# Performance work log

Hardware: AMD Instinct MI355X
Metric: run time of the kernel (lower is better)

## Reference

```python
import jax, jax.numpy as jnp
import numpy as np

B, H = 65536, 1024


def setup_inputs() -> dict:
    key = jax.random.key(0)
    ks = jax.random.split(key, 8)
    pos = jax.random.normal(ks[0], (B, 3), dtype=jnp.float32)
    quat = jax.random.normal(ks[1], (B, 4), dtype=jnp.float32)
    quat = quat / jnp.linalg.norm(quat, axis=-1, keepdims=True)
    gripper = jax.random.randint(ks[2], (B, 1), 0, 2).astype(jnp.float32)
    actions = jnp.concatenate([pos, quat, gripper], axis=-1)  # (B, 8)
    return {
        "actions": actions,
        "pos_W": jax.random.normal(ks[3], (3, H), dtype=jnp.float32) * 0.02,
        "pos_b": jnp.zeros((H,), dtype=jnp.float32),
        "rot_W": jax.random.normal(ks[4], (6, H), dtype=jnp.float32) * 0.02,
        "rot_b": jnp.zeros((H,), dtype=jnp.float32),
        "open_emb": jax.random.normal(ks[5], (2, H), dtype=jnp.float32) * 0.02,
        "ln_g": jnp.ones((H,), dtype=jnp.float32),
        "ln_b": jnp.zeros((H,), dtype=jnp.float32),
    }


def quat_to_euler_xyz(quat):
    # scipy R.from_quat uses (x, y, z, w); as_euler('xyz') = extrinsic x-y-z
    # (classic roll/pitch/yaw). Normalize like scipy does.
    quat = quat / jnp.linalg.norm(quat, axis=-1, keepdims=True)
    x, y, z, w = quat[..., 0], quat[..., 1], quat[..., 2], quat[..., 3]
    roll = jnp.arctan2(2.0 * (w * x + y * z), 1.0 - 2.0 * (x * x + y * y))
    pitch = jnp.arcsin(jnp.clip(2.0 * (w * y - z * x), -1.0, 1.0))
    yaw = jnp.arctan2(2.0 * (w * z + x * y), 1.0 - 2.0 * (y * y + z * z))
    return jnp.stack([roll, pitch, yaw], axis=-1)


def reference(actions, pos_W, pos_b, rot_W, rot_b, open_emb, ln_g, ln_b):
    pos_embeds = actions[..., :3] @ pos_W + pos_b
    open_idx = actions[..., 7].astype(jnp.int32)
    open_embeds = open_emb[open_idx]
    # original detaches quats (.data.cpu()) before conversion
    eul = quat_to_euler_xyz(jax.lax.stop_gradient(actions[..., 3:7]))
    rot_inputs = jnp.concatenate([jnp.sin(eul), jnp.cos(eul)], axis=-1)  # (B, 6)
    rot_embeds = rot_inputs @ rot_W + rot_b
    h = pos_embeds + rot_embeds + open_embeds
    mu = jnp.mean(h, axis=-1, keepdims=True)
    var = jnp.mean(jnp.square(h - mu), axis=-1, keepdims=True)
    return (h - mu) / jnp.sqrt(var + 1e-12) * ln_g + ln_b
```

## Files before the change

kernel.cpp:

```cpp
#include <hip/hip_runtime.h>
#include <math.h>


#define HDIM 1024
#define TPB  256
#define CPT  4
#define RPB  32

__global__ __launch_bounds__(TPB) void action_embed_kernel(
    const float* __restrict__ actions,
    const float* __restrict__ pos_W, const float* __restrict__ pos_b,
    const float* __restrict__ rot_W, const float* __restrict__ rot_b,
    const float* __restrict__ open_emb,
    const float* __restrict__ ln_g, const float* __restrict__ ln_b,
    float* __restrict__ out, int B)
{
    __shared__ float s_coef[RPB][12];
    __shared__ float s_red[2][4][2];

    const int tid  = threadIdx.x;
    const int col  = tid * CPT;
    const int row0 = blockIdx.x * RPB;

    const float4 wp0 = *(const float4*)(pos_W + 0 * HDIM + col);
    const float4 wp1 = *(const float4*)(pos_W + 1 * HDIM + col);
    const float4 wp2 = *(const float4*)(pos_W + 2 * HDIM + col);
    const float4 wr0 = *(const float4*)(rot_W + 0 * HDIM + col);
    const float4 wr1 = *(const float4*)(rot_W + 1 * HDIM + col);
    const float4 wr2 = *(const float4*)(rot_W + 2 * HDIM + col);
    const float4 wr3 = *(const float4*)(rot_W + 3 * HDIM + col);
    const float4 wr4 = *(const float4*)(rot_W + 4 * HDIM + col);
    const float4 wr5 = *(const float4*)(rot_W + 5 * HDIM + col);
    const float4 wo0 = *(const float4*)(open_emb + 0 * HDIM + col);
    const float4 wo1 = *(const float4*)(open_emb + 1 * HDIM + col);
    float4 bb;
    {
        float4 pb = *(const float4*)(pos_b + col);
        float4 rb = *(const float4*)(rot_b + col);
        bb = make_float4(pb.x + rb.x, pb.y + rb.y, pb.z + rb.z, pb.w + rb.w);
    }
    const float4 g  = *(const float4*)(ln_g + col);
    const float4 bt = *(const float4*)(ln_b + col);

    if (tid < RPB) {
        const int r = row0 + tid;
        if (r < B) {
            const float4 a0 = *(const float4*)(actions + (size_t)r * 8);
            const float4 a1 = *(const float4*)(actions + (size_t)r * 8 + 4);
            float qx = a0.w, qy = a1.x, qz = a1.y, qw = a1.z;
            const float n = 1.0f / sqrtf(qx * qx + qy * qy + qz * qz + qw * qw);
            qx *= n; qy *= n; qz *= n; qw *= n;
            const float sr_n = 2.0f * (qw * qx + qy * qz);
            const float cr_n = 1.0f - 2.0f * (qx * qx + qy * qy);
            float sr, cr;
            {
                const float r2 = sr_n * sr_n + cr_n * cr_n;
                if (r2 < 1e-37f) { sr = 0.0f; cr = 1.0f; }
                else { const float ri = 1.0f / sqrtf(r2); sr = sr_n * ri; cr = cr_n * ri; }
            }
            float sp = 2.0f * (qw * qy - qz * qx);
            sp = fminf(1.0f, fmaxf(-1.0f, sp));
            const float cp = sqrtf(fmaxf(0.0f, 1.0f - sp * sp));
            const float sy_n = 2.0f * (qw * qz + qx * qy);
            const float cy_n = 1.0f - 2.0f * (qy * qy + qz * qz);
            float sy, cy;
            {
                const float r2 = sy_n * sy_n + cy_n * cy_n;
                if (r2 < 1e-37f) { sy = 0.0f; cy = 1.0f; }
                else { const float ri = 1.0f / sqrtf(r2); sy = sy_n * ri; cy = cy_n * ri; }
            }
            s_coef[tid][0] = a0.x;
            s_coef[tid][1] = a0.y;
            s_coef[tid][2] = a0.z;
            s_coef[tid][3] = sr;
            s_coef[tid][4] = sp;
            s_coef[tid][5] = sy;
            s_coef[tid][6] = cr;
            s_coef[tid][7] = cp;
            s_coef[tid][8] = cy;
            int idx = (int)a1.w;
            idx = idx < 0 ? 0 : (idx > 1 ? 1 : idx);
            s_coef[tid][9] = (float)idx;
        }
    }
    __syncthreads();

    const int wave = tid >> 6;
    const int lane = tid & 63;
    const int nrows = (B - row0 < RPB) ? (B - row0) : RPB;

    for (int rr = 0; rr < nrows; ++rr) {
        const float c0 = s_coef[rr][0], c1 = s_coef[rr][1], c2 = s_coef[rr][2];
        const float sr = s_coef[rr][3], sp = s_coef[rr][4], sy = s_coef[rr][5];
        const float cr = s_coef[rr][6], cp = s_coef[rr][7], cy = s_coef[rr][8];
        const bool open = s_coef[rr][9] != 0.0f;

        float4 h;
#define COMPONENT(f)                                                        \
        {                                                                   \
            float hh = bb.f + (open ? wo1.f : wo0.f);                       \
            hh = fmaf(c0, wp0.f, hh);                                       \
            hh = fmaf(c1, wp1.f, hh);                                       \
            hh = fmaf(c2, wp2.f, hh);                                       \
            hh = fmaf(sr, wr0.f, hh);                                       \
            hh = fmaf(sp, wr1.f, hh);                                       \
            hh = fmaf(sy, wr2.f, hh);                                       \
            hh = fmaf(cr, wr3.f, hh);                                       \
            hh = fmaf(cp, wr4.f, hh);                                       \
            hh = fmaf(cy, wr5.f, hh);                                       \
            h.f = hh;                                                       \
        }
        COMPONENT(x) COMPONENT(y) COMPONENT(z) COMPONENT(w)
#undef COMPONENT

        float ps = h.x + h.y + h.z + h.w;
        float pq = h.x * h.x + h.y * h.y + h.z * h.z + h.w * h.w;
        #pragma unroll
        for (int off = 32; off > 0; off >>= 1) {
            ps += __shfl_xor(ps, off, 64);
            pq += __shfl_xor(pq, off, 64);
        }
        const int buf = rr & 1;
        if (lane == 0) {
            s_red[buf][wave][0] = ps;
            s_red[buf][wave][1] = pq;
        }
        __syncthreads();
        const float sum = s_red[buf][0][0] + s_red[buf][1][0] +
                          s_red[buf][2][0] + s_red[buf][3][0];
        const float sq  = s_red[buf][0][1] + s_red[buf][1][1] +
                          s_red[buf][2][1] + s_red[buf][3][1];

        const float mu  = sum * (1.0f / HDIM);
        float var = fmaf(sq, 1.0f / HDIM, -mu * mu);
        var = fmaxf(var, 0.0f);
        const float rstd = 1.0f / sqrtf(var + 1e-12f);

        float4 o;
        o.x = fmaf((h.x - mu) * rstd, g.x, bt.x);
        o.y = fmaf((h.y - mu) * rstd, g.y, bt.y);
        o.z = fmaf((h.z - mu) * rstd, g.z, bt.z);
        o.w = fmaf((h.w - mu) * rstd, g.w, bt.w);
        *(float4*)(out + (size_t)(row0 + rr) * HDIM + col) = o;
    }
}

extern "C" void kernel_launch(void* const* d_in, const int* in_sizes, int n_in,
                              void* d_out, int out_size, void* d_ws, size_t ws_size,
                              hipStream_t stream) {
    const float* actions  = (const float*)d_in[0];
    const float* pos_W    = (const float*)d_in[1];
    const float* pos_b    = (const float*)d_in[2];
    const float* rot_W    = (const float*)d_in[3];
    const float* rot_b    = (const float*)d_in[4];
    const float* open_emb = (const float*)d_in[5];
    const float* ln_g     = (const float*)d_in[6];
    const float* ln_b     = (const float*)d_in[7];
    float* out = (float*)d_out;

    const int B = in_sizes[0] / 8;
    const int grid = (B + RPB - 1) / RPB;
    hipLaunchKernelGGL(action_embed_kernel, dim3(grid), dim3(TPB), 0, stream,
                       actions, pos_W, pos_b, rot_W, rot_b, open_emb,
                       ln_g, ln_b, out, B);
}
```

Baseline: 289.3 us.

## Batch four rows per block-wide LayerNorm reduction and use nontemporal stores

The row loop now processes four rows per iteration. It computes all four partial sums and interleaves their wave shuffles, then does a single __syncthreads for the group instead of one barrier per row. Output writes use nontemporal stores to avoid cache pollution on the large streaming output. The open-embedding select is folded into the bias plus a difference FMA, and launch bounds request higher occupancy. The tail no longer handles row counts that are not a multiple of four, which would read stale coefficients and write past the end for such B.

```diff
diff --git a/kernel.cpp b/kernel.cpp
--- a/kernel.cpp
+++ b/kernel.cpp
@@ -2,12 +2,15 @@
 #include <math.h>
 
 
-#define HDIM 1024
-#define TPB  256
-#define CPT  4
-#define RPB  32
+#define HDIM  1024
+#define TPB   256
+#define CPT   4
+#define RPB   32
+#define BATCH 4
 
-__global__ __launch_bounds__(TPB) void action_embed_kernel(
+typedef float v4f __attribute__((ext_vector_type(4)));
+
+__global__ __launch_bounds__(TPB, 4) void action_embed_kernel(
     const float* __restrict__ actions,
     const float* __restrict__ pos_W, const float* __restrict__ pos_b,
     const float* __restrict__ rot_W, const float* __restrict__ rot_b,
@@ -15,8 +18,8 @@
     const float* __restrict__ ln_g, const float* __restrict__ ln_b,
     float* __restrict__ out, int B)
 {
-    __shared__ float s_coef[RPB][12];
-    __shared__ float s_red[2][4][2];
+    __shared__ float s_coef[RPB][10];
+    __shared__ float s_red[2][BATCH][4][2];
 
     const int tid  = threadIdx.x;
     const int col  = tid * CPT;
@@ -31,13 +34,15 @@
     const float4 wr3 = *(const float4*)(rot_W + 3 * HDIM + col);
     const float4 wr4 = *(const float4*)(rot_W + 4 * HDIM + col);
     const float4 wr5 = *(const float4*)(rot_W + 5 * HDIM + col);
-    const float4 wo0 = *(const float4*)(open_emb + 0 * HDIM + col);
-    const float4 wo1 = *(const float4*)(open_emb + 1 * HDIM + col);
-    float4 bb;
+    float4 bb, dopen;
     {
-        float4 pb = *(const float4*)(pos_b + col);
-        float4 rb = *(const float4*)(rot_b + col);
-        bb = make_float4(pb.x + rb.x, pb.y + rb.y, pb.z + rb.z, pb.w + rb.w);
+        const float4 pb = *(const float4*)(pos_b + col);
+        const float4 rb = *(const float4*)(rot_b + col);
+        const float4 o0 = *(const float4*)(open_emb + 0 * HDIM + col);
+        const float4 o1 = *(const float4*)(open_emb + 1 * HDIM + col);
+        bb    = make_float4(pb.x + rb.x + o0.x, pb.y + rb.y + o0.y,
+                            pb.z + rb.z + o0.z, pb.w + rb.w + o0.w);
+        dopen = make_float4(o1.x - o0.x, o1.y - o0.y, o1.z - o0.z, o1.w - o0.w);
     }
     const float4 g  = *(const float4*)(ln_g + col);
     const float4 bt = *(const float4*)(ln_b + col);
@@ -89,59 +94,78 @@
     const int lane = tid & 63;
     const int nrows = (B - row0 < RPB) ? (B - row0) : RPB;
 
-    for (int rr = 0; rr < nrows; ++rr) {
-        const float c0 = s_coef[rr][0], c1 = s_coef[rr][1], c2 = s_coef[rr][2];
-        const float sr = s_coef[rr][3], sp = s_coef[rr][4], sy = s_coef[rr][5];
-        const float cr = s_coef[rr][6], cp = s_coef[rr][7], cy = s_coef[rr][8];
-        const bool open = s_coef[rr][9] != 0.0f;
+    for (int rb = 0; rb < nrows; rb += BATCH) {
+        const int buf = (rb >> 2) & 1;
+        float4 h[BATCH];
+        float  ps[BATCH], pq[BATCH];
 
-        float4 h;
+        #pragma unroll
+        for (int j = 0; j < BATCH; ++j) {
+            const int rr = rb + j;
+            const float c0 = s_coef[rr][0], c1 = s_coef[rr][1], c2 = s_coef[rr][2];
+            const float sr = s_coef[rr][3], sp = s_coef[rr][4], sy = s_coef[rr][5];
+            const float cr = s_coef[rr][6], cp = s_coef[rr][7], cy = s_coef[rr][8];
+            const float op = s_coef[rr][9];
 #define COMPONENT(f)                                                        \
-        {                                                                   \
-            float hh = bb.f + (open ? wo1.f : wo0.f);                       \
-            hh = fmaf(c0, wp0.f, hh);                                       \
-            hh = fmaf(c1, wp1.f, hh);                                       \
-            hh = fmaf(c2, wp2.f, hh);                                       \
-            hh = fmaf(sr, wr0.f, hh);                                       \
-            hh = fmaf(sp, wr1.f, hh);                                       \
-            hh = fmaf(sy, wr2.f, hh);                                       \
-            hh = fmaf(cr, wr3.f, hh);                                       \
-            hh = fmaf(cp, wr4.f, hh);                                       \
-            hh = fmaf(cy, wr5.f, hh);                                       \
-            h.f = hh;                                                       \
+            {                                                               \
+                float hh = fmaf(op, dopen.f, bb.f);                         \
+                hh = fmaf(c0, wp0.f, hh);                                   \
+                hh = fmaf(c1, wp1.f, hh);                                   \
+                hh = fmaf(c2, wp2.f, hh);                                   \
+                hh = fmaf(sr, wr0.f, hh);                                   \
+                hh = fmaf(sp, wr1.f, hh);                                   \
+                hh = fmaf(sy, wr2.f, hh);                                   \
+                hh = fmaf(cr, wr3.f, hh);                                   \
+                hh = fmaf(cp, wr4.f, hh);                                   \
+                hh = fmaf(cy, wr5.f, hh);                                   \
+                h[j].f = hh;                                                \
+            }
+            COMPONENT(x) COMPONENT(y) COMPONENT(z) COMPONENT(w)
+#undef COMPONENT
+            ps[j] = (h[j].x + h[j].y) + (h[j].z + h[j].w);
+            float q = h[j].x * h[j].x;
+            q = fmaf(h[j].y, h[j].y, q);
+            q = fmaf(h[j].z, h[j].z, q);
+            q = fmaf(h[j].w, h[j].w, q);
+            pq[j] = q;
         }
-        COMPONENT(x) COMPONENT(y) COMPONENT(z) COMPONENT(w)
-#undef COMPONENT
 
-        float ps = h.x + h.y + h.z + h.w;
-        float pq = h.x * h.x + h.y * h.y + h.z * h.z + h.w * h.w;
         #pragma unroll
         for (int off = 32; off > 0; off >>= 1) {
-            ps += __shfl_xor(ps, off, 64);
-            pq += __shfl_xor(pq, off, 64);
+            #pragma unroll
+            for (int j = 0; j < BATCH; ++j) {
+                ps[j] += __shfl_xor(ps[j], off, 64);
+                pq[j] += __shfl_xor(pq[j], off, 64);
+            }
         }
-        const int buf = rr & 1;
         if (lane == 0) {
-            s_red[buf][wave][0] = ps;
-            s_red[buf][wave][1] = pq;
+            #pragma unroll
+            for (int j = 0; j < BATCH; ++j) {
+                s_red[buf][j][wave][0] = ps[j];
+                s_red[buf][j][wave][1] = pq[j];
+            }
         }
         __syncthreads();
-        const float sum = s_red[buf][0][0] + s_red[buf][1][0] +
-                          s_red[buf][2][0] + s_red[buf][3][0];
-        const float sq  = s_red[buf][0][1] + s_red[buf][1][1] +
-                          s_red[buf][2][1] + s_red[buf][3][1];
 
-        const float mu  = sum * (1.0f / HDIM);
-        float var = fmaf(sq, 1.0f / HDIM, -mu * mu);
-        var = fmaxf(var, 0.0f);
-        const float rstd = 1.0f / sqrtf(var + 1e-12f);
+        #pragma unroll
+        for (int j = 0; j < BATCH; ++j) {
+            const float4 p0 = *(const float4*)&s_red[buf][j][0][0];
+            const float4 p1 = *(const float4*)&s_red[buf][j][2][0];
+            const float sum = (p0.x + p0.z) + (p1.x + p1.z);
+            const float sq  = (p0.y + p0.w) + (p1.y + p1.w);
+            const float mu  = sum * (1.0f / HDIM);
+            float var = fmaf(sq, 1.0f / HDIM, -mu * mu);
+            var = fmaxf(var, 0.0f);
+            const float rstd = 1.0f / sqrtf(var + 1e-12f);
 
-        float4 o;
-        o.x = fmaf((h.x - mu) * rstd, g.x, bt.x);
-        o.y = fmaf((h.y - mu) * rstd, g.y, bt.y);
-        o.z = fmaf((h.z - mu) * rstd, g.z, bt.z);
-        o.w = fmaf((h.w - mu) * rstd, g.w, bt.w);
-        *(float4*)(out + (size_t)(row0 + rr) * HDIM + col) = o;
+            v4f o;
+            o.x = fmaf((h[j].x - mu) * rstd, g.x, bt.x);
+            o.y = fmaf((h[j].y - mu) * rstd, g.y, bt.y);
+            o.z = fmaf((h[j].z - mu) * rstd, g.z, bt.z);
+            o.w = fmaf((h[j].w - mu) * rstd, g.w, bt.w);
+            __builtin_nontemporal_store(o,
+                (v4f*)(out + (size_t)(row0 + rb + j) * HDIM + col));
+        }
     }
 }
 
```

After: 296.0 us. +2.3%, slower.
